# Performance work log

Measured on AMD Instinct MI355X. Metric: run time of the kernel, lower is better.

Reference implementation:

```python
import jax, jax.numpy as jnp
import numpy as np

N = 100000   # nodes
E = 1600000  # edges
F = 256      # feature_dim
H = 64       # hidden_dim == out_channels
HEADS = 1


def setup_inputs() -> dict:
    key = jax.random.key(0)
    ks = jax.random.split(key, 12)
    x = jax.random.normal(ks[0], (N, F), dtype=jnp.float32)
    edge_index = jax.random.randint(ks[1], (2, E), 0, N, dtype=jnp.int32)
    s = 0.05
    params = {
        'W_proj': jax.random.normal(ks[2], (F, H), dtype=jnp.float32) * s,
        'b_proj': jnp.zeros((H,), dtype=jnp.float32),
        'Wq1': jax.random.normal(ks[3], (H, HEADS * H), dtype=jnp.float32) * s,
        'Wk1': jax.random.normal(ks[4], (H, HEADS * H), dtype=jnp.float32) * s,
        'Wv1': jax.random.normal(ks[5], (H, HEADS * H), dtype=jnp.float32) * s,
        'Wq2': jax.random.normal(ks[6], (H, HEADS * H), dtype=jnp.float32) * s,
        'Wk2': jax.random.normal(ks[7], (H, HEADS * H), dtype=jnp.float32) * s,
        'Wv2': jax.random.normal(ks[8], (H, HEADS * H), dtype=jnp.float32) * s,
        'W_sig': jax.random.normal(ks[9], (H, 1), dtype=jnp.float32) * s,
        'b_sig': jnp.zeros((1,), dtype=jnp.float32),
    }
    return {'x': x, 'edge_index': edge_index, **params}


def _gat_layer(x, src, dst, Wq, Wk, Wv):
    # x: [N, H]; src/dst: [E] (edge_index[0]=source j, edge_index[1]=dest i)
    n = x.shape[0]
    q = (x @ Wq).reshape(n, HEADS, H)
    k = (x @ Wk).reshape(n, HEADS, H)
    v = (x @ Wv).reshape(n, HEADS, H)
    # edge-wise scores: (q_i * k_j).sum(-1) / sqrt(out_channels)
    scores = jnp.einsum('ehc,ehc->eh', q[dst], k[src]) / np.float32(np.sqrt(H))
    alpha = jax.nn.relu(scores)                                  # [E, HEADS]
    # segment softmax over destination neighborhoods (numerically stable)
    m = jax.ops.segment_max(alpha, dst, num_segments=n)          # [N, HEADS]
    m = jnp.where(jnp.isfinite(m), m, jnp.float32(0.0))
    e = jnp.exp(alpha - m[dst])
    denom = jax.ops.segment_sum(e, dst, num_segments=n)
    a = e / (denom[dst] + jnp.float32(1e-16))                    # [E, HEADS]
    # scatter-weighted sum of values to destinations
    out = jax.ops.segment_sum(v[src] * a[:, :, None], dst, num_segments=n)
    return out.mean(axis=1), a                                   # [N, H], [E, HEADS]


def reference(x, edge_index, W_proj, b_proj, Wq1, Wk1, Wv1, Wq2, Wk2, Wv2, W_sig, b_sig):
    src, dst = edge_index[0], edge_index[1]
    h = jax.nn.gelu(x @ W_proj + b_proj, approximate=False)
    h, attn1 = _gat_layer(h, src, dst, Wq1, Wk1, Wv1)
    h = jax.nn.gelu(h, approximate=False)
    h, attn2 = _gat_layer(h, src, dst, Wq2, Wk2, Wv2)
    signals = h @ W_sig + b_sig                                  # [N, 1]
    return signals, attn1, attn2
```

## Files before the change

kernel.cpp:

```cpp
#include <hip/hip_runtime.h>
#include <hip/hip_fp16.h>
#include <math.h>

#define FF 256
#define HH 64

typedef __attribute__((ext_vector_type(8))) short short8;
typedef __attribute__((ext_vector_type(4))) float f32x4;
typedef unsigned long long ull;

__device__ __forceinline__ float gelu_f(float x) {
    float ax = fabsf(x) * 0.70710678118654752f;
    float t = __builtin_amdgcn_rcpf(fmaf(0.3275911f, ax, 1.0f));
    float poly = t * fmaf(t, fmaf(t, fmaf(t, fmaf(t, 1.061405429f, -1.453152027f),
                  1.421413741f), -0.284496736f), 0.254829592f);
    float er = 1.0f - poly * __expf(-ax * ax);
    er = (x < 0.f) ? -er : er;
    return 0.5f * x * (1.0f + er);
}

__device__ __forceinline__ unsigned short bf16rne(float f) {
    unsigned u = __float_as_uint(f);
    unsigned r = u + 0x7FFFu + ((u >> 16) & 1u);
    return (unsigned short)(r >> 16);
}

__device__ __forceinline__ void bf16split(float f, short& hi, short& lo) {
    unsigned u = __float_as_uint(f);
    unsigned r = u + 0x7FFFu + ((u >> 16) & 1u);
    hi = (short)(r >> 16);
    float fh = __uint_as_float(r & 0xFFFF0000u);
    float fl = f - fh;
    unsigned u2 = __float_as_uint(fl);
    unsigned r2 = u2 + 0x7FFFu + ((u2 >> 16) & 1u);
    lo = (short)(r2 >> 16);
}

__device__ __forceinline__ __half2 shfl_xor_h2(__half2 v, int off) {
    union { __half2 h; int i; } u;
    u.h = v;
    u.i = __shfl_xor(u.i, off, 64);
    return u.h;
}

__global__ __launch_bounds__(256) void k_wprep(
        const float* __restrict__ Wp,
        const float* __restrict__ Wq1, const float* __restrict__ Wk1, const float* __restrict__ Wv1,
        const float* __restrict__ Wq2, const float* __restrict__ Wk2, const float* __restrict__ Wv2,
        short* __restrict__ wf) {
    int total = 16384 + 6 * 4096;
    for (int gid = blockIdx.x * 256 + threadIdx.x; gid < total; gid += gridDim.x * 256) {
        const float* W;
        int fid, hibase, lobase;
        if (gid < 16384) {
            W = Wp; fid = gid; hibase = 0; lobase = 16384;
        } else {
            int t = gid - 16384;
            int m = t >> 12;
            fid = t & 4095;
            switch (m) {
                case 0: W = Wq1; break;
                case 1: W = Wk1; break;
                case 2: W = Wv1; break;
                case 3: W = Wq2; break;
                case 4: W = Wk2; break;
                default: W = Wv2; break;
            }
            hibase = 32768 + m * 8192;
            lobase = hibase + 4096;
        }
        int j    = fid & 7;
        int lane = (fid >> 3) & 63;
        int ct   = (fid >> 9) & 3;
        int s    = fid >> 11;
        int k    = s * 32 + (lane >> 4) * 8 + j;
        int col  = ct * 16 + (lane & 15);
        short hi, lo;
        bf16split(W[k * HH + col], hi, lo);
        wf[hibase + fid] = hi;
        wf[lobase + fid] = lo;
    }
}


__global__ __launch_bounds__(256) void k_partA(const int* __restrict__ dst,
        int* __restrict__ blockHist, int E, int PB, int NB) {
    __shared__ int hist[256];
    int t = threadIdx.x, bid = blockIdx.x;
    hist[t] = 0;
    __syncthreads();
    int base = bid * 4096;
    int e0 = base + t * 4;
    if (base + 4095 < E) {
        #pragma unroll
        for (int i = 0; i < 4; ++i) {
            int4 d = *reinterpret_cast<const int4*>(dst + e0 + i * 1024);
            atomicAdd(&hist[d.x >> 9], 1);
            atomicAdd(&hist[d.y >> 9], 1);
            atomicAdd(&hist[d.z >> 9], 1);
            atomicAdd(&hist[d.w >> 9], 1);
        }
    } else {
        for (int i = 0; i < 4; ++i)
            for (int j = 0; j < 4; ++j) {
                int e = e0 + i * 1024 + j;
                if (e < E) atomicAdd(&hist[dst[e] >> 9], 1);
            }
    }
    __syncthreads();
    if (t < NB) blockHist[t * PB + bid] = hist[t];
}

__global__ __launch_bounds__(512) void k_partA2(int* __restrict__ blockHist,
        int* __restrict__ bucketTotal, int PB) {
    __shared__ int buf[512];
    int t = threadIdx.x, b = blockIdx.x;
    int orig = (t < PB) ? blockHist[b * PB + t] : 0;
    buf[t] = orig;
    __syncthreads();
    #pragma unroll
    for (int off = 1; off < 512; off <<= 1) {
        int v = (t >= off) ? buf[t - off] : 0;
        __syncthreads();
        buf[t] += v;
        __syncthreads();
    }
    if (t < PB) blockHist[b * PB + t] = buf[t] - orig;
    if (t == 511) bucketTotal[b] = buf[511];
}

__global__ __launch_bounds__(256) void k_partA2b(const int* __restrict__ bucketTotal,
        int* __restrict__ bucketBase, int* __restrict__ rowptr, int NB, int N, int E) {
    __shared__ int buf[256];
    int t = threadIdx.x;
    int orig = (t < NB) ? bucketTotal[t] : 0;
    buf[t] = orig;
    __syncthreads();
    #pragma unroll
    for (int off = 1; off < 256; off <<= 1) {
        int v = (t >= off) ? buf[t - off] : 0;
        __syncthreads();
        buf[t] += v;
        __syncthreads();
    }
    if (t < NB) bucketBase[t] = buf[t] - orig;
    if (t == 0) { bucketBase[NB] = buf[255]; rowptr[N] = E; }
}

__device__ __forceinline__ void do_partB3(int bid, const int* __restrict__ src,
        const int* __restrict__ dst, const int* __restrict__ blockBase,
        const int* __restrict__ bucketBase,
        ull* __restrict__ bps, int E, int PB, int NB) {
    if (bid >= PB) return;
    __shared__ int cur[256];
    int t = threadIdx.x;
    if (t < NB) cur[t] = bucketBase[t] + blockBase[t * PB + bid];
    __syncthreads();
    int base = bid * 4096;
    int e0 = base + t * 4;
    auto place = [&](int d, int s, int e) {
        int bu = d >> 9;
        int pos = atomicAdd(&cur[bu], 1);
        bps[pos] = ((ull)(d & 511) << 38) | ((ull)s << 21) | (unsigned)e;
    };
    if (base + 4095 < E) {
        #pragma unroll
        for (int i = 0; i < 4; ++i) {
            int4 d4 = *reinterpret_cast<const int4*>(dst + e0 + i * 1024);
            int4 s4 = *reinterpret_cast<const int4*>(src + e0 + i * 1024);
            int eb = e0 + i * 1024;
            place(d4.x, s4.x, eb);
            place(d4.y, s4.y, eb + 1);
            place(d4.z, s4.z, eb + 2);
            place(d4.w, s4.w, eb + 3);
        }
    } else {
        for (int i = 0; i < 4; ++i)
            for (int j = 0; j < 4; ++j) {
                int e = e0 + i * 1024 + j;
                if (e < E) place(dst[e], src[e], e);
            }
    }
}

__device__ __forceinline__ void do_partC1(int b, const ull* __restrict__ bps,
        const int* __restrict__ bucketBase,
        int* __restrict__ rowptr, int* __restrict__ esrc, int* __restrict__ posArr,
        int N, int NB) {
    if (b >= NB) return;
    __shared__ int cnt[512], sc[512], cur[512], pairbuf[256];
    int t = threadIdx.x;
    cnt[t] = 0; cnt[t + 256] = 0;
    cur[t] = 0; cur[t + 256] = 0;
    __syncthreads();
    int rB = bucketBase[b], rE = bucketBase[b + 1];
    for (int p = rB + t; p < rE; p += 256)
        atomicAdd(&cnt[(int)(bps[p] >> 38)], 1);
    __syncthreads();
    int a  = cnt[2 * t], b2 = cnt[2 * t + 1];
    int ps = a + b2;
    pairbuf[t] = ps;
    __syncthreads();
    #pragma unroll
    for (int off = 1; off < 256; off <<= 1) {
        int v = (t >= off) ? pairbuf[t - off] : 0;
        __syncthreads();
        pairbuf[t] += v;
        __syncthreads();
    }
    int pex = pairbuf[t] - ps;
    sc[2 * t]     = pex;
    sc[2 * t + 1] = pex + a;
    __syncthreads();
    int lo = b << 9;
    #pragma unroll
    for (int i = 0; i < 2; ++i) {
        int idx = t + i * 256;
        int node = lo + idx;
        if (node < N) rowptr[node] = rB + sc[idx];
    }
    for (int p = rB + t; p < rE; p += 256) {
        ull u = bps[p];
        int local = (int)(u >> 38);
        int s = (int)((u >> 21) & 0x1FFFF);
        int r = atomicAdd(&cur[local], 1);
        int pos = rB + sc[local] + r;
        esrc[pos] = s;
        posArr[p] = pos;
    }
}

__device__ __forceinline__ void do_partC2(int bid, const ull* __restrict__ bps,
        const int* __restrict__ posArr, int* __restrict__ inv, int E) {
    int p0 = (bid * 256 + threadIdx.x) * 4;
    if (p0 + 3 < E) {
        ull u0 = bps[p0], u1 = bps[p0 + 1], u2 = bps[p0 + 2], u3 = bps[p0 + 3];
        int4 ps = *reinterpret_cast<const int4*>(posArr + p0);
        inv[(int)(u0 & 0x1FFFFF)] = ps.x;
        inv[(int)(u1 & 0x1FFFFF)] = ps.y;
        inv[(int)(u2 & 0x1FFFFF)] = ps.z;
        inv[(int)(u3 & 0x1FFFFF)] = ps.w;
    } else {
        for (int p = p0; p < E; ++p)
            inv[(int)(bps[p] & 0x1FFFFF)] = posArr[p];
    }
}

__device__ __forceinline__ void do_attn(int bid, const float* __restrict__ ecsr,
        const int* __restrict__ inv, float* __restrict__ attn, int E) {
    int e0 = (bid * 256 + threadIdx.x) * 4;
    if (e0 + 3 < E) {
        int4 i4 = *reinterpret_cast<const int4*>(inv + e0);
        float4 a;
        a.x = ecsr[i4.x]; a.y = ecsr[i4.y]; a.z = ecsr[i4.z]; a.w = ecsr[i4.w];
        *reinterpret_cast<float4*>(attn + e0) = a;
    } else {
        for (int e = e0; e < E; ++e) attn[e] = ecsr[inv[e]];
    }
}

__device__ __forceinline__ void do_proj(int bid, const float* __restrict__ x,
        const short* __restrict__ wf, const float* __restrict__ b,
        float* __restrict__ h, int n) {
    if (bid * 64 >= n) return;
    int lane = threadIdx.x & 63;
    int w    = threadIdx.x >> 6;
    int m    = lane & 15, g = lane >> 4;
    int rowc = min(bid * 64 + w * 16 + m, n - 1);
    const float* xrow = x + (size_t)rowc * FF + g * 8;
    const short* wlo = wf + 16384;
    f32x4 acc[4];
    #pragma unroll
    for (int ct = 0; ct < 4; ++ct) acc[ct] = (f32x4){0.f, 0.f, 0.f, 0.f};
    #pragma unroll
    for (int s = 0; s < 8; ++s) {
        float4 a0 = *reinterpret_cast<const float4*>(xrow + s * 32);
        float4 a1 = *reinterpret_cast<const float4*>(xrow + s * 32 + 4);
        float av[8] = {a0.x, a0.y, a0.z, a0.w, a1.x, a1.y, a1.z, a1.w};
        short8 ah, al;
        #pragma unroll
        for (int j = 0; j < 8; ++j) { short hi, lo; bf16split(av[j], hi, lo); ah[j] = hi; al[j] = lo; }
        #pragma unroll
        for (int ct = 0; ct < 4; ++ct) {
            int fo = ((s * 4 + ct) * 64 + lane) * 8;
            short8 bh = *reinterpret_cast<const short8*>(wf + fo);
            short8 bl = *reinterpret_cast<const short8*>(wlo + fo);
            acc[ct] = __builtin_amdgcn_mfma_f32_16x16x32_bf16(ah, bh, acc[ct], 0, 0, 0);
            acc[ct] = __builtin_amdgcn_mfma_f32_16x16x32_bf16(al, bh, acc[ct], 0, 0, 0);
            acc[ct] = __builtin_amdgcn_mfma_f32_16x16x32_bf16(ah, bl, acc[ct], 0, 0, 0);
        }
    }
    int orow0 = bid * 64 + w * 16 + g * 4;
    #pragma unroll
    for (int ct = 0; ct < 4; ++ct) {
        int col = ct * 16 + m;
        float bias = b[col];
        #pragma unroll
        for (int r = 0; r < 4; ++r) {
            int row = orow0 + r;
            if (row < n) h[(size_t)row * HH + col] = acc[ct][r] + bias;
        }
    }
}

__device__ __forceinline__ void do_qkv(int bid, const float* __restrict__ hsrc,
        const short* __restrict__ wfq, const short* __restrict__ wfk, const short* __restrict__ wfv,
        __half* __restrict__ qh, __half* __restrict__ kv, int n) {
    if (bid * 64 >= n) return;
    int lane = threadIdx.x & 63;
    int w    = threadIdx.x >> 6;
    int m    = lane & 15, g = lane >> 4;
    int rowc = min(bid * 64 + w * 16 + m, n - 1);
    const float* hrow = hsrc + (size_t)rowc * HH + g * 8;
    f32x4 aq[4], ak[4], av_[4];
    #pragma unroll
    for (int ct = 0; ct < 4; ++ct) {
        aq[ct] = (f32x4){0.f, 0.f, 0.f, 0.f};
        ak[ct] = (f32x4){0.f, 0.f, 0.f, 0.f};
        av_[ct] = (f32x4){0.f, 0.f, 0.f, 0.f};
    }
    #pragma unroll
    for (int s = 0; s < 2; ++s) {
        float4 a0 = *reinterpret_cast<const float4*>(hrow + s * 32);
        float4 a1 = *reinterpret_cast<const float4*>(hrow + s * 32 + 4);
        float avv[8] = {a0.x, a0.y, a0.z, a0.w, a1.x, a1.y, a1.z, a1.w};
        short8 ah;
        #pragma unroll
        for (int j = 0; j < 8; ++j) ah[j] = (short)bf16rne(gelu_f(avv[j]));
        #pragma unroll
        for (int ct = 0; ct < 4; ++ct) {
            int fo = ((s * 4 + ct) * 64 + lane) * 8;
            short8 qh8 = *reinterpret_cast<const short8*>(wfq + fo);
            short8 ql8 = *reinterpret_cast<const short8*>(wfq + 4096 + fo);
            short8 kh8 = *reinterpret_cast<const short8*>(wfk + fo);
            short8 kl8 = *reinterpret_cast<const short8*>(wfk + 4096 + fo);
            short8 vh8 = *reinterpret_cast<const short8*>(wfv + fo);
            short8 vl8 = *reinterpret_cast<const short8*>(wfv + 4096 + fo);
            aq[ct] = __builtin_amdgcn_mfma_f32_16x16x32_bf16(ah, qh8, aq[ct], 0, 0, 0);
            aq[ct] = __builtin_amdgcn_mfma_f32_16x16x32_bf16(ah, ql8, aq[ct], 0, 0, 0);
            ak[ct] = __builtin_amdgcn_mfma_f32_16x16x32_bf16(ah, kh8, ak[ct], 0, 0, 0);
            ak[ct] = __builtin_amdgcn_mfma_f32_16x16x32_bf16(ah, kl8, ak[ct], 0, 0, 0);
            av_[ct] = __builtin_amdgcn_mfma_f32_16x16x32_bf16(ah, vh8, av_[ct], 0, 0, 0);
            av_[ct] = __builtin_amdgcn_mfma_f32_16x16x32_bf16(ah, vl8, av_[ct], 0, 0, 0);
        }
    }
    int orow0 = bid * 64 + w * 16 + g * 4;
    #pragma unroll
    for (int ct = 0; ct < 4; ++ct) {
        int col = ct * 16 + m;
        int cb  = (col >> 3) * 16 + (col & 7);
        #pragma unroll
        for (int r = 0; r < 4; ++r) {
            int row = orow0 + r;
            if (row < n) {
                qh[(size_t)row * HH + col]     = __float2half(aq[ct][r]);
                kv[(size_t)row * 128 + cb]     = __float2half(ak[ct][r]);
                kv[(size_t)row * 128 + cb + 8] = __float2half(av_[ct][r]);
            }
        }
    }
}

template<bool LAST>
__device__ __forceinline__ void do_edge(int ebid,
        const __half* __restrict__ qarr, const __half* __restrict__ kv,
        const int* __restrict__ rowptr,
        const int* __restrict__ esrc,
        float* __restrict__ ecsr,
        float* __restrict__ hout,
        float* __restrict__ signals,
        const float* __restrict__ Wsig, const float* __restrict__ bsig,
        int n) {
    int node = ebid * 4 + (threadIdx.x >> 6);
    if (node >= n) return;
    int lane = threadIdx.x & 63;
    int li = lane & 7, g = lane >> 3;
    int start = rowptr[node], end = rowptr[node + 1];
    int deg = end - start;
    __half2 q2[4];
    {
        union { uint4 u; __half2 h[4]; } Q;
        Q.u = *reinterpret_cast<const uint4*>(qarr + (size_t)node * HH + li * 8);
        #pragma unroll
        for (int j = 0; j < 4; ++j) q2[j] = Q.h[j];
    }
    int p0 = start + lane;
    int el = (p0 < end) ? esrc[p0] : 0;

    __half2 acc2[4];
    #pragma unroll
    for (int j = 0; j < 4; ++j) acc2[j] = __float2half2_rn(0.f);
    float s = 0.f;
    for (int c = 0; c < deg; c += 16) {
        int idx0 = c + g, idx1 = c + 8 + g;
        bool v0 = idx0 < deg, v1 = idx1 < deg;
        int sv0, sv1;
        if (c + 16 <= 64) {
            sv0 = __shfl(el, idx0);
            sv1 = __shfl(el, idx1);
        } else {
            sv0 = v0 ? esrc[start + idx0] : 0;
            sv1 = v1 ? esrc[start + idx1] : 0;
        }
        const __half* b0 = kv + (size_t)sv0 * 128 + li * 16;
        const __half* b1 = kv + (size_t)sv1 * 128 + li * 16;
        union { uint4 u; __half2 h[4]; } K0, V0, K1, V1;
        K0.u = *reinterpret_cast<const uint4*>(b0);
        V0.u = *reinterpret_cast<const uint4*>(b0 + 8);
        K1.u = *reinterpret_cast<const uint4*>(b1);
        V1.u = *reinterpret_cast<const uint4*>(b1 + 8);
        __half2 d20 = __float2half2_rn(0.f);
        __half2 d21 = __float2half2_rn(0.f);
        #pragma unroll
        for (int j = 0; j < 4; ++j) {
            d20 = __hfma2(q2[j], K0.h[j], d20);
            d21 = __hfma2(q2[j], K1.h[j], d21);
        }
        float d0 = __low2float(d20) + __high2float(d20);
        float d1 = __low2float(d21) + __high2float(d21);
        d0 += __shfl_xor(d0, 1); d1 += __shfl_xor(d1, 1);
        d0 += __shfl_xor(d0, 2); d1 += __shfl_xor(d1, 2);
        d0 += __shfl_xor(d0, 4); d1 += __shfl_xor(d1, 4);
        float e0 = v0 ? __expf(fmaxf(d0 * 0.125f, 0.f)) : 0.f;
        float e1 = v1 ? __expf(fmaxf(d1 * 0.125f, 0.f)) : 0.f;
        s += e0 + e1;
        if (v0 && li == 0) ecsr[start + idx0] = e0;
        if (v1 && li == 0) ecsr[start + idx1] = e1;
        __half2 e20 = __float2half2_rn(e0);
        __half2 e21 = __float2half2_rn(e1);
        #pragma unroll
        for (int j = 0; j < 4; ++j) {
            acc2[j] = __hfma2(e20, V0.h[j], acc2[j]);
            acc2[j] = __hfma2(e21, V1.h[j], acc2[j]);
        }
    }
    #pragma unroll
    for (int off = 8; off < 64; off <<= 1) {
        s += __shfl_xor(s, off);
        #pragma unroll
        for (int j = 0; j < 4; ++j)
            acc2[j] = __hadd2(acc2[j], shfl_xor_h2(acc2[j], off));
    }
    float inv = 1.0f / (s + 1e-16f);
    float af[8];
    #pragma unroll
    for (int j = 0; j < 4; ++j) {
        af[2 * j]     = __low2float(acc2[j]);
        af[2 * j + 1] = __high2float(acc2[j]);
    }

    if (!LAST) {
        if (g == 0) {
            float4 o0, o1;
            o0.x = af[0] * inv; o0.y = af[1] * inv; o0.z = af[2] * inv; o0.w = af[3] * inv;
            o1.x = af[4] * inv; o1.y = af[5] * inv; o1.z = af[6] * inv; o1.w = af[7] * inv;
            *reinterpret_cast<float4*>(hout + (size_t)node * HH + li * 8)     = o0;
            *reinterpret_cast<float4*>(hout + (size_t)node * HH + li * 8 + 4) = o1;
        }
    } else {
        float4 w0 = *reinterpret_cast<const float4*>(Wsig + li * 8);
        float4 w1 = *reinterpret_cast<const float4*>(Wsig + li * 8 + 4);
        float t = af[0] * w0.x + af[1] * w0.y + af[2] * w0.z + af[3] * w0.w
                + af[4] * w1.x + af[5] * w1.y + af[6] * w1.z + af[7] * w1.w;
        t *= inv;
        t += __shfl_xor(t, 1);
        t += __shfl_xor(t, 2);
        t += __shfl_xor(t, 4);
        if (lane == 0) signals[node] = t + bsig[0];
    }
    for (int p = p0; p < end; p += 64)
        ecsr[p] *= inv;
}

__global__ __launch_bounds__(256) void k_proj_partB3(
        const float* __restrict__ x, const short* __restrict__ wf,
        const float* __restrict__ b, float* __restrict__ h, int n,
        const int* __restrict__ src, const int* __restrict__ dst,
        const int* __restrict__ blockBase, const int* __restrict__ bucketBase,
        ull* __restrict__ bps, int E, int PB, int NB) {
    int bid = blockIdx.x >> 1;
    if ((blockIdx.x & 1) == 0) do_proj(bid, x, wf, b, h, n);
    else                       do_partB3(bid, src, dst, blockBase, bucketBase, bps, E, PB, NB);
}

__global__ __launch_bounds__(256) void k_qkv_partC1(
        const float* __restrict__ hsrc,
        const short* __restrict__ wfq, const short* __restrict__ wfk, const short* __restrict__ wfv,
        __half* __restrict__ qh, __half* __restrict__ kv, int n,
        const ull* __restrict__ bps, const int* __restrict__ bucketBase,
        int* __restrict__ rowptr, int* __restrict__ esrc, int* __restrict__ posArr, int NB) {
    int bid = blockIdx.x >> 1;
    if ((blockIdx.x & 1) == 0) do_qkv(bid, hsrc, wfq, wfk, wfv, qh, kv, n);
    else                       do_partC1(bid, bps, bucketBase, rowptr, esrc, posArr, n, NB);
}

__global__ __launch_bounds__(256) void k_edge1_partC2(
        const __half* __restrict__ qarr, const __half* __restrict__ kv,
        const int* __restrict__ rowptr, const int* __restrict__ esrc,
        float* __restrict__ ecsr, float* __restrict__ hout, int n,
        const ull* __restrict__ bps, const int* __restrict__ posArr,
        int* __restrict__ inv, int E, int C2B) {
    int bid = blockIdx.x >> 1;
    if ((blockIdx.x & 1) == 0)
        do_edge<false>(bid, qarr, kv, rowptr, esrc, ecsr, hout, nullptr, nullptr, nullptr, n);
    else if (bid < C2B)
        do_partC2(bid, bps, posArr, inv, E);
}

__global__ __launch_bounds__(256) void k_qkv_attn(
        const float* __restrict__ hsrc,
        const short* __restrict__ wfq, const short* __restrict__ wfk, const short* __restrict__ wfv,
        __half* __restrict__ qh, __half* __restrict__ kv, int n,
        const float* __restrict__ ecsr, const int* __restrict__ inv,
        float* __restrict__ attn, int E) {
    int bid = blockIdx.x >> 1;
    if ((blockIdx.x & 1) == 0) do_qkv(bid, hsrc, wfq, wfk, wfv, qh, kv, n);
    else                       do_attn(bid, ecsr, inv, attn, E);
}

__global__ __launch_bounds__(256) void k_edge2(
        const __half* __restrict__ qarr, const __half* __restrict__ kv,
        const int* __restrict__ rowptr, const int* __restrict__ esrc,
        float* __restrict__ ecsr, float* __restrict__ signals,
        const float* __restrict__ Wsig, const float* __restrict__ bsig, int n) {
    do_edge<true>(blockIdx.x, qarr, kv, rowptr, esrc, ecsr, nullptr, signals, Wsig, bsig, n);
}

__global__ __launch_bounds__(256) void k_attn(const float* __restrict__ ecsr,
        const int* __restrict__ inv, float* __restrict__ attn, int E) {
    do_attn(blockIdx.x, ecsr, inv, attn, E);
}

extern "C" void kernel_launch(void* const* d_in, const int* in_sizes, int n_in,
                              void* d_out, int out_size, void* d_ws, size_t ws_size,
                              hipStream_t stream) {
    const float* x   = (const float*)d_in[0];
    const int*   ei  = (const int*)  d_in[1];
    const float* Wp  = (const float*)d_in[2];
    const float* bp  = (const float*)d_in[3];
    const float* Wq1 = (const float*)d_in[4];
    const float* Wk1 = (const float*)d_in[5];
    const float* Wv1 = (const float*)d_in[6];
    const float* Wq2 = (const float*)d_in[7];
    const float* Wk2 = (const float*)d_in[8];
    const float* Wv2 = (const float*)d_in[9];
    const float* Wsg = (const float*)d_in[10];
    const float* bsg = (const float*)d_in[11];

    const int N = in_sizes[0] / FF;
    const int E = in_sizes[1] / 2;
    const int* src = ei;
    const int* dst = ei + E;

    const int NB = (N + 511) >> 9;
    const int PB = (E + 4095) >> 12;

    char* ws = (char*)d_ws;
    size_t off = 0;
    auto alloc = [&](size_t bytes) -> void* {
        void* p = ws + off;
        off += (bytes + 255) & ~(size_t)255;
        return p;
    };
    __half* qh   = (__half*)alloc((size_t)N * HH * 2);
    __half* kv   = (__half*)alloc((size_t)N * 128 * 2);
    float* h     = (float*)alloc((size_t)N * HH * 4);
    float* ecsr  = (float*)alloc((size_t)E * 4);
    int* inv     = (int*)alloc((size_t)E * 4);
    int* esrc    = (int*)alloc((size_t)E * 4);
    int* posArr  = (int*)alloc((size_t)E * 4);
    ull* bps     = (ull*)alloc((size_t)E * 8);
    int* rowptr  = (int*)alloc((size_t)(N + 1) * 4);
    int* blockHist   = (int*)alloc((size_t)NB * PB * 4);
    int* bucketTotal = (int*)alloc((size_t)NB * 4);
    int* bucketBase  = (int*)alloc((size_t)(NB + 1) * 4);
    short* wf    = (short*)alloc((size_t)81920 * 2);

    float* out     = (float*)d_out;
    float* signals = out;
    float* attn1   = out + N;
    float* attn2   = out + N + E;

    k_wprep<<<64, 256, 0, stream>>>(Wp, Wq1, Wk1, Wv1, Wq2, Wk2, Wv2, wf);

    k_partA<<<PB, 256, 0, stream>>>(dst, blockHist, E, PB, NB);
    k_partA2<<<NB, 512, 0, stream>>>(blockHist, bucketTotal, PB);
    k_partA2b<<<1, 256, 0, stream>>>(bucketTotal, bucketBase, rowptr, NB, N, E);

    int gemmBlocks = (N + 63) / 64;
    int e4Blocks   = ((E + 3) / 4 + 255) / 256;
    int edgeBlocks = (N + 3) / 4;

    int f1 = 2 * max(gemmBlocks, PB);
    k_proj_partB3<<<f1, 256, 0, stream>>>(x, wf, bp, h, N,
            src, dst, blockHist, bucketBase, bps, E, PB, NB);

    const short* wfbase = wf + 32768;
    int f2 = 2 * max(gemmBlocks, NB);
    k_qkv_partC1<<<f2, 256, 0, stream>>>(h, wfbase, wfbase + 8192, wfbase + 16384,
            qh, kv, N, bps, bucketBase, rowptr, esrc, posArr, NB);

    int f3 = 2 * max(edgeBlocks, e4Blocks);
    k_edge1_partC2<<<f3, 256, 0, stream>>>(qh, kv, rowptr, esrc, ecsr, h, N,
            bps, posArr, inv, E, e4Blocks);

    int f4 = 2 * max(gemmBlocks, e4Blocks);
    k_qkv_attn<<<f4, 256, 0, stream>>>(h, wfbase + 24576, wfbase + 32768, wfbase + 40960,
            qh, kv, N, ecsr, inv, attn1, E);

    k_edge2<<<edgeBlocks, 256, 0, stream>>>(qh, kv, rowptr, esrc, ecsr,
            signals, Wsg, bsg, N);
    k_attn<<<e4Blocks, 256, 0, stream>>>(ecsr, inv, attn2, E);
}
```

Before: 333.9 us.

## Write inverse permutation in CSR build and defer softmax normalization to attn gather

The CSR bucket pass now writes the edge-to-CSR inverse index directly, which removes the posArr buffer and the separate partC2 scatter pass. The edge kernels no longer rescale the per-edge exp values in place. Instead they store one reciprocal denominator per node, and the attention-output gather multiplies by it, fetched through dst. This drops a read-modify-write over the E-length ecsr array and an E-length intermediate, at the cost of an extra dst load and random dnode gathers in the attn pass. The first edge kernel now runs standalone rather than fused with partC2.

```diff
diff --git a/kernel.cpp b/kernel.cpp
--- a/kernel.cpp
+++ b/kernel.cpp
@@ -185,7 +185,7 @@
 
 __device__ __forceinline__ void do_partC1(int b, const ull* __restrict__ bps,
         const int* __restrict__ bucketBase,
-        int* __restrict__ rowptr, int* __restrict__ esrc, int* __restrict__ posArr,
+        int* __restrict__ rowptr, int* __restrict__ esrc, int* __restrict__ inv,
         int N, int NB) {
     if (b >= NB) return;
     __shared__ int cnt[512], sc[512], cur[512], pairbuf[256];
@@ -226,36 +226,25 @@
         int r = atomicAdd(&cur[local], 1);
         int pos = rB + sc[local] + r;
         esrc[pos] = s;
-        posArr[p] = pos;
-    }
-}
-
-__device__ __forceinline__ void do_partC2(int bid, const ull* __restrict__ bps,
-        const int* __restrict__ posArr, int* __restrict__ inv, int E) {
-    int p0 = (bid * 256 + threadIdx.x) * 4;
-    if (p0 + 3 < E) {
-        ull u0 = bps[p0], u1 = bps[p0 + 1], u2 = bps[p0 + 2], u3 = bps[p0 + 3];
-        int4 ps = *reinterpret_cast<const int4*>(posArr + p0);
-        inv[(int)(u0 & 0x1FFFFF)] = ps.x;
-        inv[(int)(u1 & 0x1FFFFF)] = ps.y;
-        inv[(int)(u2 & 0x1FFFFF)] = ps.z;
-        inv[(int)(u3 & 0x1FFFFF)] = ps.w;
-    } else {
-        for (int p = p0; p < E; ++p)
-            inv[(int)(bps[p] & 0x1FFFFF)] = posArr[p];
+        inv[(int)(u & 0x1FFFFF)] = pos;
     }
 }
 
 __device__ __forceinline__ void do_attn(int bid, const float* __restrict__ ecsr,
-        const int* __restrict__ inv, float* __restrict__ attn, int E) {
+        const int* __restrict__ inv, const float* __restrict__ dnode,
+        const int* __restrict__ dst, float* __restrict__ attn, int E) {
     int e0 = (bid * 256 + threadIdx.x) * 4;
     if (e0 + 3 < E) {
         int4 i4 = *reinterpret_cast<const int4*>(inv + e0);
+        int4 d4 = *reinterpret_cast<const int4*>(dst + e0);
         float4 a;
-        a.x = ecsr[i4.x]; a.y = ecsr[i4.y]; a.z = ecsr[i4.z]; a.w = ecsr[i4.w];
+        a.x = ecsr[i4.x] * dnode[d4.x];
+        a.y = ecsr[i4.y] * dnode[d4.y];
+        a.z = ecsr[i4.z] * dnode[d4.z];
+        a.w = ecsr[i4.w] * dnode[d4.w];
         *reinterpret_cast<float4*>(attn + e0) = a;
     } else {
-        for (int e = e0; e < E; ++e) attn[e] = ecsr[inv[e]];
+        for (int e = e0; e < E; ++e) attn[e] = ecsr[inv[e]] * dnode[dst[e]];
     }
 }
 
@@ -362,16 +351,17 @@
 }
 
 template<bool LAST>
-__device__ __forceinline__ void do_edge(int ebid,
+__global__ __launch_bounds__(256) void k_edge(
         const __half* __restrict__ qarr, const __half* __restrict__ kv,
         const int* __restrict__ rowptr,
         const int* __restrict__ esrc,
         float* __restrict__ ecsr,
+        float* __restrict__ dnode,
         float* __restrict__ hout,
         float* __restrict__ signals,
         const float* __restrict__ Wsig, const float* __restrict__ bsig,
         int n) {
-    int node = ebid * 4 + (threadIdx.x >> 6);
+    int node = blockIdx.x * 4 + (threadIdx.x >> 6);
     if (node >= n) return;
     int lane = threadIdx.x & 63;
     int li = lane & 7, g = lane >> 3;
@@ -442,6 +432,7 @@
             acc2[j] = __hadd2(acc2[j], shfl_xor_h2(acc2[j], off));
     }
     float inv = 1.0f / (s + 1e-16f);
+    if (lane == 0) dnode[node] = inv;
     float af[8];
     #pragma unroll
     for (int j = 0; j < 4; ++j) {
@@ -468,8 +459,6 @@
         t += __shfl_xor(t, 4);
         if (lane == 0) signals[node] = t + bsig[0];
     }
-    for (int p = p0; p < end; p += 64)
-        ecsr[p] *= inv;
 }
 
 __global__ __launch_bounds__(256) void k_proj_partB3(
@@ -488,23 +477,10 @@
         const short* __restrict__ wfq, const short* __restrict__ wfk, const short* __restrict__ wfv,
         __half* __restrict__ qh, __half* __restrict__ kv, int n,
         const ull* __restrict__ bps, const int* __restrict__ bucketBase,
-        int* __restrict__ rowptr, int* __restrict__ esrc, int* __restrict__ posArr, int NB) {
+        int* __restrict__ rowptr, int* __restrict__ esrc, int* __restrict__ inv, int NB) {
     int bid = blockIdx.x >> 1;
     if ((blockIdx.x & 1) == 0) do_qkv(bid, hsrc, wfq, wfk, wfv, qh, kv, n);
-    else                       do_partC1(bid, bps, bucketBase, rowptr, esrc, posArr, n, NB);
-}
-
-__global__ __launch_bounds__(256) void k_edge1_partC2(
-        const __half* __restrict__ qarr, const __half* __restrict__ kv,
-        const int* __restrict__ rowptr, const int* __restrict__ esrc,
-        float* __restrict__ ecsr, float* __restrict__ hout, int n,
-        const ull* __restrict__ bps, const int* __restrict__ posArr,
-        int* __restrict__ inv, int E, int C2B) {
-    int bid = blockIdx.x >> 1;
-    if ((blockIdx.x & 1) == 0)
-        do_edge<false>(bid, qarr, kv, rowptr, esrc, ecsr, hout, nullptr, nullptr, nullptr, n);
-    else if (bid < C2B)
-        do_partC2(bid, bps, posArr, inv, E);
+    else                       do_partC1(bid, bps, bucketBase, rowptr, esrc, inv, n, NB);
 }
 
 __global__ __launch_bounds__(256) void k_qkv_attn(
@@ -512,23 +488,17 @@
         const short* __restrict__ wfq, const short* __restrict__ wfk, const short* __restrict__ wfv,
         __half* __restrict__ qh, __half* __restrict__ kv, int n,
         const float* __restrict__ ecsr, const int* __restrict__ inv,
+        const float* __restrict__ dnode, const int* __restrict__ dst,
         float* __restrict__ attn, int E) {
     int bid = blockIdx.x >> 1;
     if ((blockIdx.x & 1) == 0) do_qkv(bid, hsrc, wfq, wfk, wfv, qh, kv, n);
-    else                       do_attn(bid, ecsr, inv, attn, E);
-}
-
-__global__ __launch_bounds__(256) void k_edge2(
-        const __half* __restrict__ qarr, const __half* __restrict__ kv,
-        const int* __restrict__ rowptr, const int* __restrict__ esrc,
-        float* __restrict__ ecsr, float* __restrict__ signals,
-        const float* __restrict__ Wsig, const float* __restrict__ bsig, int n) {
-    do_edge<true>(blockIdx.x, qarr, kv, rowptr, esrc, ecsr, nullptr, signals, Wsig, bsig, n);
+    else                       do_attn(bid, ecsr, inv, dnode, dst, attn, E);
 }
 
 __global__ __launch_bounds__(256) void k_attn(const float* __restrict__ ecsr,
-        const int* __restrict__ inv, float* __restrict__ attn, int E) {
-    do_attn(blockIdx.x, ecsr, inv, attn, E);
+        const int* __restrict__ inv, const float* __restrict__ dnode,
+        const int* __restrict__ dst, float* __restrict__ attn, int E) {
+    do_attn(blockIdx.x, ecsr, inv, dnode, dst, attn, E);
 }
 
 extern "C" void kernel_launch(void* const* d_in, const int* in_sizes, int n_in,
@@ -568,7 +538,7 @@
     float* ecsr  = (float*)alloc((size_t)E * 4);
     int* inv     = (int*)alloc((size_t)E * 4);
     int* esrc    = (int*)alloc((size_t)E * 4);
-    int* posArr  = (int*)alloc((size_t)E * 4);
+    float* dnode = (float*)alloc((size_t)N * 4);
     ull* bps     = (ull*)alloc((size_t)E * 8);
     int* rowptr  = (int*)alloc((size_t)(N + 1) * 4);
     int* blockHist   = (int*)alloc((size_t)NB * PB * 4);
@@ -598,17 +568,16 @@
     const short* wfbase = wf + 32768;
     int f2 = 2 * max(gemmBlocks, NB);
     k_qkv_partC1<<<f2, 256, 0, stream>>>(h, wfbase, wfbase + 8192, wfbase + 16384,
-            qh, kv, N, bps, bucketBase, rowptr, esrc, posArr, NB);
-
-    int f3 = 2 * max(edgeBlocks, e4Blocks);
-    k_edge1_partC2<<<f3, 256, 0, stream>>>(qh, kv, rowptr, esrc, ecsr, h, N,
-            bps, posArr, inv, E, e4Blocks);
+            qh, kv, N, bps, bucketBase, rowptr, esrc, inv, NB);
+
+    k_edge<false><<<edgeBlocks, 256, 0, stream>>>(qh, kv, rowptr, esrc,
+            ecsr, dnode, h, nullptr, nullptr, nullptr, N);
 
     int f4 = 2 * max(gemmBlocks, e4Blocks);
     k_qkv_attn<<<f4, 256, 0, stream>>>(h, wfbase + 24576, wfbase + 32768, wfbase + 40960,
-            qh, kv, N, ecsr, inv, attn1, E);
-
-    k_edge2<<<edgeBlocks, 256, 0, stream>>>(qh, kv, rowptr, esrc, ecsr,
-            signals, Wsg, bsg, N);
-    k_attn<<<e4Blocks, 256, 0, stream>>>(ecsr, inv, attn2, E);
-}
+            qh, kv, N, ecsr, inv, dnode, dst, attn1, E);
+
+    k_edge<true><<<edgeBlocks, 256, 0, stream>>>(qh, kv, rowptr, esrc,
+            ecsr, dnode, nullptr, signals, Wsg, bsg, N);
+    k_attn<<<e4Blocks, 256, 0, stream>>>(ecsr, inv, dnode, dst, attn2, E);
+}
```

After: 307.8 us. 1.08x faster.
